# Kernel optimization log

Measured on AMD Instinct MI355X. Metric: run time of the kernel, lower is better.

## Reference

```python
import math
import jax, jax.numpy as jnp
import numpy as np

L, NH, DF = 4, 4, 32  # num_layers, num_heads, head_dim (H=128)
EPS = 1e-5


def ln(x, g, b):
    m = x.mean(-1, keepdims=True)
    v = ((x - m) ** 2).mean(-1, keepdims=True)
    return (x - m) * jax.lax.rsqrt(v + EPS) * g + b


def mha(x, w_in, b_in, w_out, b_out):
    # torch nn.MultiheadAttention self-attention, batch_first, no mask
    B, S, H = x.shape
    q, k, v = jnp.split(x @ w_in + b_in, 3, axis=-1)
    q = q.reshape(B, S, NH, DF)
    k = k.reshape(B, S, NH, DF)
    v = v.reshape(B, S, NH, DF)
    s = jnp.einsum('bqhd,bkhd->bhqk', q, k) / math.sqrt(DF)
    a = jax.nn.softmax(s, axis=-1)
    o = jnp.einsum('bhqk,bkhd->bqhd', a, v).reshape(B, S, H)
    return o @ w_out + b_out


def _forward(X_k, time_embed, step_embed, W_tr, b_tr, W_in, b_in, g_in, be_in,
             W_e, b_e, aw, ab, ow, ob, tng, tnb, f1w, f1b, f2w, f2b, fng, fnb,
             Wq, Wk, Wv, Wo, bo, Wem, bem, Wea, bea, e1w, e1b, e2w, e2b,
             gng, gnb, eng, enb, W_out, b_out, k_index, edge_index):
    B, N, T1, Cin = X_k.shape
    H = W_in.shape[1]
    # --- precompute_graph: self-loops + structural edge features ---
    loop = jnp.arange(N, dtype=edge_index.dtype)
    ei = jnp.concatenate([edge_index, jnp.stack([loop, loop])], axis=1)
    dst, src = ei[0], ei[1]
    E = ei.shape[1]
    deg = jnp.zeros((N,), jnp.float32).at[dst].add(1.0)
    deg_max = jnp.maximum(deg.max(), 1.0)
    edge_w = 1.0 / jnp.maximum(deg[dst], 1.0)
    feat = jnp.stack([edge_w, deg[src] / deg_max, deg[dst] / deg_max], axis=1)  # [E,3]
    # --- input embedding ---
    t_emb = time_embed  # [T1, te] (lookup of arange(T1) = whole table)
    X = jnp.concatenate(
        [X_k, jnp.broadcast_to(t_emb[None, None], (B, N, T1, t_emb.shape[-1]))], axis=-1)
    h = ln(X @ W_in + b_in, g_in, be_in)
    h = h + step_embed[k_index][:, None, None, :]
    e = feat @ W_e + b_e                       # [E, de]
    t_re = t_emb @ W_tr + b_tr                 # [T1, H]
    BT = B * T1
    for l in range(L):
        # temporal attention over T1
        h_flat = h.reshape(B * N, T1, H)
        attn_out = mha(h_flat, aw[l], ab[l], ow[l], ob[l])
        h = ln(h + attn_out.reshape(B, N, T1, H), tng[l], tnb[l])
        ffn = jax.nn.gelu(h @ f1w[l] + f1b[l], approximate=False) @ f2w[l] + f2b[l]
        h = ln(h + ffn, fng[l], fnb[l])
        h = h + t_re[None, None]
        # DiGress GT sparse graph block over N
        h_BT = h.transpose(0, 2, 1, 3).reshape(BT, N, H)
        Q = (h_BT @ Wq[l]).reshape(BT, N, NH, DF)
        K = (h_BT @ Wk[l]).reshape(BT, N, NH, DF)
        V = (h_BT @ Wv[l]).reshape(BT, N, NH, DF)
        scores = (Q[:, dst] * K[:, src]).sum(-1) / math.sqrt(DF)  # [BT,E,NH]
        scores = scores * (e @ Wem[l] + bem[l] + 1.0) + (e @ Wea[l] + bea[l])
        s_max = jax.lax.stop_gradient(scores.max(axis=1, keepdims=True))
        exp_s = jnp.exp(scores - s_max)
        denom = jnp.zeros((BT, N, NH), exp_s.dtype).at[:, dst, :].add(exp_s)
        attn = exp_s / (denom[:, dst, :] + 1e-9)
        agg = (attn[..., None] * V[:, src]).reshape(BT, E, H)
        out = jnp.zeros((BT, N, H), h.dtype).at[:, dst, :].add(agg)
        h_BT = h_BT + out @ Wo[l] + bo[l]
        h_mean = jax.lax.stop_gradient(h_BT).mean(0)               # [N,H]
        e_in = jnp.concatenate([h_mean[dst], h_mean[src], e], axis=-1)
        e_mlp = jax.nn.gelu(e_in @ e1w[l] + e1b[l], approximate=False) @ e2w[l] + e2b[l]
        e = ln(e + e_mlp, eng[l], enb[l])
        h = ln(h_BT.reshape(B, T1, N, H).transpose(0, 2, 1, 3), gng[l], gnb[l])
    return jax.nn.softmax(h @ W_out + b_out, axis=-1)


def setup_inputs() -> dict:
    key = jax.random.key(0)
    B, N, T1 = 2, 2000, 12
    sd, cc, te, H, de, nh = 4, 2, 16, 128, 16, 4
    Cin = (1 + cc) * sd  # 12
    E0, max_steps = 32000, 1024
    ks = iter(jax.random.split(key, 60))
    def rn(*shape, s=0.05):
        return jax.random.normal(next(ks), shape, jnp.float32) * s
    z = lambda *s: jnp.zeros(s, jnp.float32)
    o = lambda *s: jnp.ones(s, jnp.float32)
    return dict(
        X_k=jax.random.normal(next(ks), (B, N, T1, Cin), jnp.float32),
        time_embed=rn(T1, te), step_embed=rn(max_steps, H),
        W_tr=rn(te, H), b_tr=z(H),
        W_in=rn(Cin + te, H), b_in=z(H), g_in=o(H), be_in=z(H),
        W_e=rn(3, de), b_e=z(de),
        aw=rn(L, H, 3 * H), ab=z(L, 3 * H), ow=rn(L, H, H), ob=z(L, H),
        tng=o(L, H), tnb=z(L, H),
        f1w=rn(L, H, 2 * H), f1b=z(L, 2 * H), f2w=rn(L, 2 * H, H), f2b=z(L, H),
        fng=o(L, H), fnb=z(L, H),
        Wq=rn(L, H, H), Wk=rn(L, H, H), Wv=rn(L, H, H),
        Wo=rn(L, H, H), bo=z(L, H),
        Wem=rn(L, de, nh), bem=z(L, nh), Wea=rn(L, de, nh), bea=z(L, nh),
        e1w=rn(L, 2 * H + de, 4 * de), e1b=z(L, 4 * de),
        e2w=rn(L, 4 * de, de), e2b=z(L, de),
        gng=o(L, H), gnb=z(L, H), eng=o(L, de), enb=z(L, de),
        W_out=rn(H, sd), b_out=z(sd),
        k_index=jax.random.randint(next(ks), (B,), 0, max_steps),
        edge_index=jax.random.randint(next(ks), (2, E0), 0, N),
    )


def reference(X_k, time_embed, step_embed, W_tr, b_tr, W_in, b_in, g_in, be_in,
              W_e, b_e, aw, ab, ow, ob, tng, tnb, f1w, f1b, f2w, f2b, fng, fnb,
              Wq, Wk, Wv, Wo, bo, Wem, bem, Wea, bea, e1w, e1b, e2w, e2b,
              gng, gnb, eng, enb, W_out, b_out, k_index, edge_index):
    return _forward(X_k, time_embed, step_embed, W_tr, b_tr, W_in, b_in, g_in, be_in,
                    W_e, b_e, aw, ab, ow, ob, tng, tnb, f1w, f1b, f2w, f2b, fng, fnb,
                    Wq, Wk, Wv, Wo, bo, Wem, bem, Wea, bea, e1w, e1b, e2w, e2b,
                    gng, gnb, eng, enb, W_out, b_out, k_index, edge_index)
```

## Files before the change

kernel.cpp:

```cpp
#include <hip/hip_runtime.h>
#include <math.h>

#define NN 2000
#define T1C 12
#define BBC 2
#define HHC 128
#define NHD 4
#define DFD 32
#define LLC 4
#define DEC 16
#define TEC 16
#define CINC 12
#define E0C 32000
#define EEC 34000
#define BTC 24
#define MROWS 48000
#define EPSLN 1e-5f
#define SCALEQK 0.17677669529663687f

typedef __attribute__((ext_vector_type(8))) short short8;
typedef __attribute__((ext_vector_type(4))) float f32x4;


__device__ __forceinline__ unsigned short f2b(float f)
{
    unsigned u = __float_as_uint(f);
    return (unsigned short)((u + 0x7FFF + ((u >> 16) & 1)) >> 16);
}

__device__ __forceinline__ float b2f(unsigned short h)
{
    return __uint_as_float(((unsigned)h) << 16);
}


__global__ __launch_bounds__(256) void convwp_k(const float* __restrict__ W, unsigned short* __restrict__ Bp,
                                                int LN_, int K, int N, int noff, int Ntot)
{
    int idx = blockIdx.x * blockDim.x + threadIdx.x;
    int total = LN_ * K * N;
    if (idx >= total) return;
    int l = idx / (K * N);
    int r = idx - l * (K * N);
    int k = r / N;
    int n = r - k * N + noff;
    size_t off = (size_t)l * K * Ntot +
                 ((size_t)((n >> 4) * (K >> 5) + (k >> 5)) << 9) +
                 (((k >> 3) & 3) << 7) + ((n & 15) << 3) + (k & 7);
    Bp[off] = f2b(W[idx]);
}

__global__ __launch_bounds__(256) void convw12_k(const float* __restrict__ e1w, unsigned short* __restrict__ W12P)
{
    int idx = blockIdx.x * blockDim.x + threadIdx.x;
    if (idx >= LLC * 128 * 128) return;
    int l = idx >> 14;
    int r = idx & 16383;
    int c = r >> 7, k = r & 127;
    int sk = (c < 64) ? k : k + 128;
    int sc = c & 63;
    W12P[idx] = f2b(e1w[((size_t)l * 272 + sk) * 64 + sc]);
}

__global__ __launch_bounds__(256) void convwoT_k(const float* __restrict__ Wo, unsigned short* __restrict__ WoT)
{
    int idx = blockIdx.x * blockDim.x + threadIdx.x;
    if (idx >= LLC * 128 * 128) return;
    int l = idx >> 14;
    int r = idx & 16383;
    int c = r >> 7, k = r & 127;
    WoT[idx] = f2b(Wo[((size_t)l * 128 + k) * 128 + c]);
}


template<int K, int EPI, int OUTM>
__global__ __launch_bounds__(256) void gemm2_k(
    const unsigned short* __restrict__ A, const unsigned short* __restrict__ Bp,
    const float* __restrict__ bias, float* __restrict__ C, unsigned short* __restrict__ Cb,
    const float* __restrict__ res, const float* __restrict__ gam, const float* __restrict__ bet,
    const float* __restrict__ trep,
    int M, int Ntot)
{
    __shared__ unsigned short A_s[128 * 16 * 8];
    __shared__ float red2[2][128][2];

    int tid = threadIdx.x;
    int w = tid >> 6, lane = tid & 63;
    int wr = w & 1, wc = w >> 1;
    int quad = lane >> 4, lr = lane & 15;

    const unsigned short* abase = A + (size_t)blockIdx.x * 128 * K;
    int ntg0 = blockIdx.y * 8 + wc * 4;

    f32x4 acc[4][4];
#pragma unroll
    for (int mt = 0; mt < 4; mt++)
#pragma unroll
        for (int nt = 0; nt < 4; nt++) acc[mt][nt] = (f32x4){0.f, 0.f, 0.f, 0.f};

#pragma unroll
    for (int kb = 0; kb < K; kb += 128) {
        if (kb) __syncthreads();
#pragma unroll
        for (int j = 0; j < 8; j++) {
            int s = j * 256 + tid;
            int row = s >> 4, ks = s & 15;
            int ko = ks ^ (row & 15);
            uint4 d = *(const uint4*)(abase + (size_t)row * K + kb + ko * 8);
            *(uint4*)(A_s + s * 8) = d;
        }
        __syncthreads();
#pragma unroll
        for (int k0 = 0; k0 < 128; k0 += 32) {
            short8 af[4], bf[4];
#pragma unroll
            for (int mt = 0; mt < 4; mt++) {
                int row_l = wr * 64 + mt * 16 + lr;
                int koct = (k0 >> 3) + quad;
                int slot = row_l * 16 + (koct ^ lr);
                af[mt] = *(const short8*)(A_s + slot * 8);
            }
#pragma unroll
            for (int nt = 0; nt < 4; nt++) {
                size_t off = ((size_t)(ntg0 + nt) * (K >> 5) + ((kb + k0) >> 5)) * 512 + lane * 8;
                bf[nt] = *(const short8*)(Bp + off);
            }
#pragma unroll
            for (int mt = 0; mt < 4; mt++)
#pragma unroll
                for (int nt = 0; nt < 4; nt++)
                    acc[mt][nt] = __builtin_amdgcn_mfma_f32_16x16x32_bf16(af[mt], bf[nt], acc[mt][nt], 0, 0, 0);
        }
    }

    int rbase = blockIdx.x * 128 + wr * 64;
    int cbase = blockIdx.y * 128 + wc * 64;

    if constexpr (EPI != 3 && EPI != 4 && EPI != 5) {
#pragma unroll
        for (int mt = 0; mt < 4; mt++) {
#pragma unroll
            for (int nt = 0; nt < 4; nt++) {
                int colg = cbase + nt * 16 + lr;
                float bv = bias ? bias[colg] : 0.f;
#pragma unroll
                for (int i = 0; i < 4; i++) {
                    int row = rbase + mt * 16 + quad * 4 + i;
                    float x = acc[mt][nt][i] + bv;
                    if constexpr (EPI == 1) x = 0.5f * x * (1.f + erff(x * 0.70710678118654752f));
                    if constexpr (EPI == 2) x = res[(size_t)row * Ntot + colg] + x;
                    if constexpr (OUTM & 1) C[(size_t)row * Ntot + colg] = x;
                    if constexpr (OUTM & 4)
                        Cb[(size_t)blockIdx.y * M * 128 + (size_t)row * 128 + (wc * 64 + nt * 16 + lr)] = f2b(x);
                    else if constexpr (OUTM & 2)
                        Cb[(size_t)row * Ntot + colg] = f2b(x);
                }
            }
        }
    } else {
        float s[4][4], s2l[4][4];
#pragma unroll
        for (int mt = 0; mt < 4; mt++)
#pragma unroll
            for (int i = 0; i < 4; i++) { s[mt][i] = 0.f; s2l[mt][i] = 0.f; }
#pragma unroll
        for (int mt = 0; mt < 4; mt++) {
#pragma unroll
            for (int nt = 0; nt < 4; nt++) {
                int colg = cbase + nt * 16 + lr;
                float bv = bias[colg];
#pragma unroll
                for (int i = 0; i < 4; i++) {
                    int row = rbase + mt * 16 + quad * 4 + i;
                    float x = acc[mt][nt][i] + bv + res[(size_t)row * 128 + colg];
                    acc[mt][nt][i] = x;
                    s[mt][i] += x;
                    s2l[mt][i] += x * x;
                }
            }
        }
#pragma unroll
        for (int m = 1; m < 16; m <<= 1) {
#pragma unroll
            for (int mt = 0; mt < 4; mt++)
#pragma unroll
                for (int i = 0; i < 4; i++) {
                    s[mt][i]  += __shfl_xor(s[mt][i], m, 64);
                    s2l[mt][i] += __shfl_xor(s2l[mt][i], m, 64);
                }
        }
        if (lr == 0) {
#pragma unroll
            for (int mt = 0; mt < 4; mt++)
#pragma unroll
                for (int i = 0; i < 4; i++) {
                    int rl = wr * 64 + mt * 16 + quad * 4 + i;
                    red2[wc][rl][0] = s[mt][i];
                    red2[wc][rl][1] = s2l[mt][i];
                }
        }
        __syncthreads();
#pragma unroll
        for (int mt = 0; mt < 4; mt++) {
#pragma unroll
            for (int i = 0; i < 4; i++) {
                int rl = wr * 64 + mt * 16 + quad * 4 + i;
                float st  = red2[0][rl][0] + red2[1][rl][0];
                float s2t = red2[0][rl][1] + red2[1][rl][1];
                float mu = st * (1.f / 128.f);
                float rstd = rsqrtf(s2t * (1.f / 128.f) - mu * mu + EPSLN);
                int row = rbase + mt * 16 + quad * 4 + i;
                if constexpr (EPI == 4) {
                    int t = row % T1C;
                    int bn = row / T1C;
                    int b = bn / NN;
                    int n = bn - b * NN;
                    size_t rowp = (size_t)(b * T1C + t) * NN + n;
                    const float* trow = trep + t * HHC;
#pragma unroll
                    for (int nt = 0; nt < 4; nt++) {
                        int colg = cbase + nt * 16 + lr;
                        float y = (acc[mt][nt][i] - mu) * rstd * gam[colg] + bet[colg] + trow[colg];
                        C[rowp * 128 + colg] = y;
                        Cb[rowp * 128 + colg] = f2b(y);
                    }
                } else if constexpr (EPI == 5) {
                    int bt = row / NN, n = row - bt * NN;
                    int b = bt / T1C, t = bt - b * T1C;
                    size_t rowp = ((size_t)(b * NN + n)) * T1C + t;
#pragma unroll
                    for (int nt = 0; nt < 4; nt++) {
                        int colg = cbase + nt * 16 + lr;
                        float y = (acc[mt][nt][i] - mu) * rstd * gam[colg] + bet[colg];
                        C[rowp * 128 + colg] = y;
                        Cb[rowp * 128 + colg] = f2b(y);
                    }
                } else {
#pragma unroll
                    for (int nt = 0; nt < 4; nt++) {
                        int colg = cbase + nt * 16 + lr;
                        float y = (acc[mt][nt][i] - mu) * rstd * gam[colg] + bet[colg];
                        if constexpr (OUTM & 1) C[(size_t)row * 128 + colg] = y;
                        if constexpr (OUTM & 2) Cb[(size_t)row * 128 + colg] = f2b(y);
                    }
                }
            }
        }
    }
}

template<int K, int EPI, int OUTM>
static void run_gemm2(const unsigned short* A, const unsigned short* Bp, const float* bias,
                      float* C, unsigned short* Cb, const float* res, const float* g, const float* be,
                      const float* trep, int M, int Ntot, hipStream_t stream)
{
    dim3 grid(M / 128, Ntot / 128);
    gemm2_k<K, EPI, OUTM><<<grid, 256, 0, stream>>>(A, Bp, bias, C, Cb, res, g, be, trep, M, Ntot);
}


__global__ __launch_bounds__(256) void offn_k(
    const unsigned short* __restrict__ A,
    const unsigned short* __restrict__ Wp,
    const float* __restrict__ ob_l,
    const float* __restrict__ resh,
    const float* __restrict__ tng_l, const float* __restrict__ tnb_l,
    const unsigned short* __restrict__ F1p,
    const unsigned short* __restrict__ F2p,
    const float* __restrict__ f1b_l, const float* __restrict__ f2b_l,
    const float* __restrict__ fng_l, const float* __restrict__ fnb_l,
    const float* __restrict__ trep,
    float* __restrict__ C, unsigned short* __restrict__ Cb)
{
    __shared__ unsigned short A_s[32 * 16 * 8];
    __shared__ unsigned short M_s[32 * 16 * 8];
    __shared__ float red2[2][32][2];

    int tid = threadIdx.x;
    int w = tid >> 6, lane = tid & 63;
    int wr = w & 1, wc = w >> 1;
    int quad = lane >> 4, lr = lane & 15;

    const unsigned short* abase = A + (size_t)blockIdx.x * 32 * 128;

#pragma unroll
    for (int j = 0; j < 2; j++) {
        int s = j * 256 + tid;
        int row = s >> 4, ks = s & 15;
        int ko = ks ^ (row & 15);
        uint4 d = *(const uint4*)(abase + (size_t)row * 128 + ko * 8);
        *(uint4*)(A_s + s * 8) = d;
    }
    __syncthreads();

    f32x4 wacc[4];
#pragma unroll
    for (int nt = 0; nt < 4; nt++) wacc[nt] = (f32x4){0.f, 0.f, 0.f, 0.f};
#pragma unroll
    for (int k0 = 0; k0 < 128; k0 += 32) {
        int row_l = wr * 16 + lr;
        int koct = (k0 >> 3) + quad;
        int slot = row_l * 16 + (koct ^ lr);
        short8 af = *(const short8*)(A_s + slot * 8);
        short8 bf[4];
#pragma unroll
        for (int nt = 0; nt < 4; nt++) {
            size_t off = ((size_t)(wc * 4 + nt) * 4 + (k0 >> 5)) * 512 + lane * 8;
            bf[nt] = *(const short8*)(Wp + off);
        }
#pragma unroll
        for (int nt = 0; nt < 4; nt++)
            wacc[nt] = __builtin_amdgcn_mfma_f32_16x16x32_bf16(af, bf[nt], wacc[nt], 0, 0, 0);
    }

    int rbase = blockIdx.x * 32 + wr * 16;
    int cbase = wc * 64;

    float yv[4][4];
    {
        float s1[4], s2v[4];
#pragma unroll
        for (int i = 0; i < 4; i++) { s1[i] = 0.f; s2v[i] = 0.f; }
#pragma unroll
        for (int nt = 0; nt < 4; nt++) {
            int colg = cbase + nt * 16 + lr;
            float bv = ob_l[colg];
#pragma unroll
            for (int i = 0; i < 4; i++) {
                int row = rbase + quad * 4 + i;
                float x = wacc[nt][i] + bv + resh[(size_t)row * 128 + colg];
                yv[nt][i] = x;
                s1[i] += x;
                s2v[i] += x * x;
            }
        }
#pragma unroll
        for (int m = 1; m < 16; m <<= 1) {
#pragma unroll
            for (int i = 0; i < 4; i++) {
                s1[i]  += __shfl_xor(s1[i], m, 64);
                s2v[i] += __shfl_xor(s2v[i], m, 64);
            }
        }
        if (lr == 0) {
#pragma unroll
            for (int i = 0; i < 4; i++) {
                int rl = wr * 16 + quad * 4 + i;
                red2[wc][rl][0] = s1[i];
                red2[wc][rl][1] = s2v[i];
            }
        }
        __syncthreads();
#pragma unroll
        for (int i = 0; i < 4; i++) {
            int rl = wr * 16 + quad * 4 + i;
            float st  = red2[0][rl][0] + red2[1][rl][0];
            float s2t = red2[0][rl][1] + red2[1][rl][1];
            float mu = st * (1.f / 128.f);
            float rstd = rsqrtf(s2t * (1.f / 128.f) - mu * mu + EPSLN);
            int row = wr * 16 + quad * 4 + i;
#pragma unroll
            for (int nt = 0; nt < 4; nt++) {
                int col = cbase + nt * 16 + lr;
                float y = (yv[nt][i] - mu) * rstd * tng_l[col] + tnb_l[col];
                yv[nt][i] = y;
                int cchunk = col >> 3, celem = col & 7;
                int ks = cchunk ^ (row & 15);
                A_s[(row * 16 + ks) * 8 + celem] = f2b(y);
            }
        }
    }
    __syncthreads();

    f32x4 facc[4];
#pragma unroll
    for (int nt = 0; nt < 4; nt++) facc[nt] = (f32x4){0.f, 0.f, 0.f, 0.f};

#pragma unroll
    for (int half = 0; half < 2; half++) {
        f32x4 macc[4];
#pragma unroll
        for (int nt = 0; nt < 4; nt++) macc[nt] = (f32x4){0.f, 0.f, 0.f, 0.f};
#pragma unroll
        for (int k0 = 0; k0 < 128; k0 += 32) {
            int row_l = wr * 16 + lr;
            int koct = (k0 >> 3) + quad;
            int slot = row_l * 16 + (koct ^ lr);
            short8 af = *(const short8*)(A_s + slot * 8);
            short8 bf[4];
#pragma unroll
            for (int nt = 0; nt < 4; nt++) {
                size_t off = ((size_t)(half * 8 + wc * 4 + nt) * 4 + (k0 >> 5)) * 512 + lane * 8;
                bf[nt] = *(const short8*)(F1p + off);
            }
#pragma unroll
            for (int nt = 0; nt < 4; nt++)
                macc[nt] = __builtin_amdgcn_mfma_f32_16x16x32_bf16(af, bf[nt], macc[nt], 0, 0, 0);
        }
        if (half) __syncthreads();
#pragma unroll
        for (int nt = 0; nt < 4; nt++) {
            int col = wc * 64 + nt * 16 + lr;
            float bv = f1b_l[half * 128 + col];
            int cchunk = col >> 3, celem = col & 7;
#pragma unroll
            for (int i = 0; i < 4; i++) {
                int row = wr * 16 + quad * 4 + i;
                float x = macc[nt][i] + bv;
                x = 0.5f * x * (1.f + erff(x * 0.70710678118654752f));
                int ks = cchunk ^ (row & 15);
                M_s[(row * 16 + ks) * 8 + celem] = f2b(x);
            }
        }
        __syncthreads();
#pragma unroll
        for (int k0 = 0; k0 < 128; k0 += 32) {
            int row_l = wr * 16 + lr;
            int koct = (k0 >> 3) + quad;
            int slot = row_l * 16 + (koct ^ lr);
            short8 af = *(const short8*)(M_s + slot * 8);
            short8 bf[4];
#pragma unroll
            for (int nt = 0; nt < 4; nt++) {
                size_t off = ((size_t)(wc * 4 + nt) * 8 + ((half * 128 + k0) >> 5)) * 512 + lane * 8;
                bf[nt] = *(const short8*)(F2p + off);
            }
#pragma unroll
            for (int nt = 0; nt < 4; nt++)
                facc[nt] = __builtin_amdgcn_mfma_f32_16x16x32_bf16(af, bf[nt], facc[nt], 0, 0, 0);
        }
    }

    float s[4], s2l[4];
#pragma unroll
    for (int i = 0; i < 4; i++) { s[i] = 0.f; s2l[i] = 0.f; }
#pragma unroll
    for (int nt = 0; nt < 4; nt++) {
        int colg = cbase + nt * 16 + lr;
        float bv = f2b_l[colg];
#pragma unroll
        for (int i = 0; i < 4; i++) {
            float x = facc[nt][i] + bv + yv[nt][i];
            facc[nt][i] = x;
            s[i] += x;
            s2l[i] += x * x;
        }
    }
#pragma unroll
    for (int m = 1; m < 16; m <<= 1) {
#pragma unroll
        for (int i = 0; i < 4; i++) {
            s[i]  += __shfl_xor(s[i], m, 64);
            s2l[i] += __shfl_xor(s2l[i], m, 64);
        }
    }
    if (lr == 0) {
#pragma unroll
        for (int i = 0; i < 4; i++) {
            int rl = wr * 16 + quad * 4 + i;
            red2[wc][rl][0] = s[i];
            red2[wc][rl][1] = s2l[i];
        }
    }
    __syncthreads();
#pragma unroll
    for (int i = 0; i < 4; i++) {
        int rl = wr * 16 + quad * 4 + i;
        float st  = red2[0][rl][0] + red2[1][rl][0];
        float s2t = red2[0][rl][1] + red2[1][rl][1];
        float mu = st * (1.f / 128.f);
        float rstd = rsqrtf(s2t * (1.f / 128.f) - mu * mu + EPSLN);
        int row = rbase + quad * 4 + i;
        int t = row % T1C;
        int bn = row / T1C;
        int b = bn / NN;
        int n = bn - b * NN;
        size_t rowp = (size_t)(b * T1C + t) * NN + n;
        const float* trow = trep + t * HHC;
#pragma unroll
        for (int nt = 0; nt < 4; nt++) {
            int colg = cbase + nt * 16 + lr;
            float y = (facc[nt][i] - mu) * rstd * fng_l[colg] + fnb_l[colg] + trow[colg];
            C[rowp * 128 + colg] = y;
            Cb[rowp * 128 + colg] = f2b(y);
        }
    }
}


template<int NT>
__global__ __launch_bounds__(256) void gemm_mfma_k(
    const unsigned short* __restrict__ A, const unsigned short* __restrict__ WT,
    float* __restrict__ C, int M, int K)
{
    const int Nc = NT * 32;
    int tid = threadIdx.x;
    int w = tid >> 6, lane = tid & 63;
    int wr = w & 1, wc = w >> 1;
    int r0 = blockIdx.x * 32 + wr * 16;
    int c0 = wc * NT * 16;
    int lr = lane & 15;
    int kq = (lane >> 4) * 8;
    int arow = r0 + lr; if (arow >= M) arow = M - 1;
    const unsigned short* ap = A + (size_t)arow * K + kq;
    const unsigned short* wp = WT + (size_t)(c0 + lr) * K + kq;

    f32x4 acc[NT];
#pragma unroll
    for (int t = 0; t < NT; t++) acc[t] = (f32x4){0.f, 0.f, 0.f, 0.f};

    for (int k0 = 0; k0 < K; k0 += 32) {
        short8 a = *(const short8*)(ap + k0);
#pragma unroll
        for (int t = 0; t < NT; t++) {
            short8 b = *(const short8*)(wp + (size_t)t * 16 * K + k0);
            acc[t] = __builtin_amdgcn_mfma_f32_16x16x32_bf16(a, b, acc[t], 0, 0, 0);
        }
    }

    int orow0 = r0 + (lane >> 4) * 4;
#pragma unroll
    for (int t = 0; t < NT; t++) {
        int col = c0 + t * 16 + lr;
#pragma unroll
        for (int i = 0; i < 4; i++) {
            int row = orow0 + i;
            if (row < M) C[(size_t)row * Nc + col] = acc[t][i];
        }
    }
}

__global__ __launch_bounds__(256) void gemm_hm_k(
    const unsigned short* __restrict__ A, const unsigned short* __restrict__ WT,
    const float* __restrict__ mA, const float* __restrict__ bo,
    unsigned short* __restrict__ hmb, int M, int K)
{
    const int NT = 4;
    int tid = threadIdx.x;
    int w = tid >> 6, lane = tid & 63;
    int wr = w & 1, wc = w >> 1;
    int r0 = blockIdx.x * 32 + wr * 16;
    int c0 = wc * NT * 16;
    int lr = lane & 15;
    int kq = (lane >> 4) * 8;
    int arow = r0 + lr; if (arow >= M) arow = M - 1;
    const unsigned short* ap = A + (size_t)arow * K + kq;
    const unsigned short* wp = WT + (size_t)(c0 + lr) * K + kq;

    f32x4 acc[NT];
#pragma unroll
    for (int t = 0; t < NT; t++) acc[t] = (f32x4){0.f, 0.f, 0.f, 0.f};

    for (int k0 = 0; k0 < K; k0 += 32) {
        short8 a = *(const short8*)(ap + k0);
#pragma unroll
        for (int t = 0; t < NT; t++) {
            short8 b = *(const short8*)(wp + (size_t)t * 16 * K + k0);
            acc[t] = __builtin_amdgcn_mfma_f32_16x16x32_bf16(a, b, acc[t], 0, 0, 0);
        }
    }

    int orow0 = r0 + (lane >> 4) * 4;
#pragma unroll
    for (int t = 0; t < NT; t++) {
        int col = c0 + t * 16 + lr;
#pragma unroll
        for (int i = 0; i < 4; i++) {
            int row = orow0 + i;
            if (row < M) {
                float x = acc[t][i] + mA[(size_t)row * 128 + col] + bo[col];
                hmb[(size_t)row * 128 + col] = f2b(x);
            }
        }
    }
}


__global__ __launch_bounds__(256) void emlp_k(const float* __restrict__ P12,
                                              const int* __restrict__ dst, const int* __restrict__ src,
                                              const float* __restrict__ e1wE, const float* __restrict__ e1b_l,
                                              const float* __restrict__ e2w_l, const float* __restrict__ e2b_l,
                                              const float* __restrict__ g, const float* __restrict__ be,
                                              float* __restrict__ e)
{
    __shared__ float tl[4][64];
    int wv = threadIdx.x >> 6, l = threadIdx.x & 63;
    int r = blockIdx.x * 4 + wv;
    int d = dst[r], s = src[r];
    const float* ep = e + (size_t)r * DEC;
    float t = P12[(size_t)d * 128 + l] + P12[(size_t)s * 128 + 64 + l] + e1b_l[l];
#pragma unroll
    for (int k = 0; k < DEC; k++) t += ep[k] * e1wE[k * 64 + l];
    t = 0.5f * t * (1.f + erff(t * 0.70710678118654752f));
    tl[wv][l] = t;
    __syncthreads();
    int c = l & 15, kq = l >> 4;
    float p = 0.f;
#pragma unroll
    for (int j = 0; j < 16; j++) p += tl[wv][kq * 16 + j] * e2w_l[(kq * 16 + j) * 16 + c];
    p += __shfl_xor(p, 16, 64);
    p += __shfl_xor(p, 32, 64);
    float x = p + e2b_l[c] + ep[c];
    float s1 = x, s2 = x * x;
#pragma unroll
    for (int m = 1; m < 16; m <<= 1) {
        s1 += __shfl_xor(s1, m, 64);
        s2 += __shfl_xor(s2, m, 64);
    }
    float mu = s1 * (1.f / 16.f);
    float rstd = rsqrtf(s2 * (1.f / 16.f) - mu * mu + EPSLN);
    float y = (x - mu) * rstd * g[c] + be[c];
    if (l < 16) e[(size_t)r * DEC + c] = y;
}


__global__ __launch_bounds__(256) void zero_deg_k(int* __restrict__ degi)
{
    int i = blockIdx.x * blockDim.x + threadIdx.x;
    if (i < NN) degi[i] = 0;
}

__global__ __launch_bounds__(256) void build_edges_k(const int* __restrict__ eidx,
                                                     int* __restrict__ dst, int* __restrict__ src,
                                                     int* __restrict__ degi)
{
    int e = blockIdx.x * blockDim.x + threadIdx.x;
    if (e >= EEC) return;
    int d, s;
    if (e < E0C) { d = eidx[e]; s = eidx[E0C + e]; }
    else { d = e - E0C; s = e - E0C; }
    dst[e] = d;
    src[e] = s;
    atomicAdd(&degi[d], 1);
}

__global__ __launch_bounds__(256) void scan_k(const int* __restrict__ degi, int* __restrict__ rowptr,
                                              int* __restrict__ cursor, float* __restrict__ degmaxf)
{
    __shared__ int ssum[256];
    __shared__ int smx[256];
    int tid = threadIdx.x;
    int vals[8];
    int s = 0, mx = 0;
    int base = tid * 8;
#pragma unroll
    for (int j = 0; j < 8; j++) {
        int idx = base + j;
        int v = (idx < NN) ? degi[idx] : 0;
        vals[j] = v; s += v; mx = max(mx, v);
    }
    ssum[tid] = s; smx[tid] = mx;
    __syncthreads();
    for (int off = 1; off < 256; off <<= 1) {
        int t = (tid >= off) ? ssum[tid - off] : 0;
        __syncthreads();
        ssum[tid] += t;
        __syncthreads();
    }
    for (int off = 128; off > 0; off >>= 1) {
        if (tid < off) smx[tid] = max(smx[tid], smx[tid + off]);
        __syncthreads();
    }
    if (tid == 0) *degmaxf = fmaxf((float)smx[0], 1.f);
    int running = ssum[tid] - s;
#pragma unroll
    for (int j = 0; j < 8; j++) {
        int idx = base + j;
        if (idx < NN) { rowptr[idx] = running; cursor[idx] = running; running += vals[j]; }
    }
    if (tid == 255) rowptr[NN] = ssum[255];
}

__global__ __launch_bounds__(256) void feat_k(const int* __restrict__ dst, const int* __restrict__ src,
                                              const int* __restrict__ degi, const float* __restrict__ degmaxf,
                                              int* __restrict__ cursor, int* __restrict__ srcCSR,
                                              int* __restrict__ epos,
                                              const float* __restrict__ We, const float* __restrict__ bE,
                                              float* __restrict__ e)
{
    int ei = blockIdx.x * blockDim.x + threadIdx.x;
    if (ei >= EEC) return;
    int d = dst[ei], s = src[ei];
    int pos = atomicAdd(&cursor[d], 1);
    srcCSR[pos] = s;
    epos[ei] = pos;
    float dm = *degmaxf;
    float degd = (float)degi[d], degs = (float)degi[s];
    float f0 = 1.f / fmaxf(degd, 1.f);
    float f1 = degs / dm, f2 = degd / dm;
#pragma unroll
    for (int c = 0; c < DEC; c++)
        e[ei * DEC + c] = bE[c] + f0 * We[c] + f1 * We[DEC + c] + f2 * We[2 * DEC + c];
}


__global__ __launch_bounds__(256) void embed_k(const float* __restrict__ Xk, const float* __restrict__ temb,
                                               const float* __restrict__ Win, const float* __restrict__ bin,
                                               const float* __restrict__ g, const float* __restrict__ be,
                                               const float* __restrict__ stepemb, const int* __restrict__ kidx,
                                               float* __restrict__ h, unsigned short* __restrict__ hb)
{
    int row = blockIdx.x * 4 + (threadIdx.x >> 6);
    int l = threadIdx.x & 63;
    int t = row % T1C;
    int bn = row / T1C;
    int b = bn / NN;
    const float* xk = Xk + (size_t)row * CINC;
    const float* tp = temb + t * TEC;
    float acc0 = bin[l], acc1 = bin[l + 64];
#pragma unroll
    for (int k = 0; k < CINC; k++) {
        float xv = xk[k];
        acc0 += xv * Win[k * HHC + l];
        acc1 += xv * Win[k * HHC + l + 64];
    }
#pragma unroll
    for (int k = 0; k < TEC; k++) {
        float xv = tp[k];
        acc0 += xv * Win[(CINC + k) * HHC + l];
        acc1 += xv * Win[(CINC + k) * HHC + l + 64];
    }
    float s = acc0 + acc1, s2 = acc0 * acc0 + acc1 * acc1;
#pragma unroll
    for (int m = 32; m >= 1; m >>= 1) {
        s  += __shfl_xor(s, m, 64);
        s2 += __shfl_xor(s2, m, 64);
    }
    float mu = s * (1.f / 128.f);
    float rstd = rsqrtf(s2 * (1.f / 128.f) - mu * mu + EPSLN);
    const float* se = stepemb + (size_t)kidx[b] * HHC;
    float v0 = (acc0 - mu) * rstd * g[l] + be[l] + se[l];
    float v1 = (acc1 - mu) * rstd * g[l + 64] + be[l + 64] + se[l + 64];
    size_t ob = (size_t)row * HHC;
    h[ob + l] = v0;
    h[ob + l + 64] = v1;
    hb[ob + l] = f2b(v0);
    hb[ob + l + 64] = f2b(v1);
}

__global__ __launch_bounds__(128) void tre_k(const float* __restrict__ temb, const float* __restrict__ Wtr,
                                             const float* __restrict__ btr, float* __restrict__ tre)
{
    int t = blockIdx.x, c = threadIdx.x;
    float acc = btr[c];
#pragma unroll
    for (int k = 0; k < TEC; k++) acc += temb[t * TEC + k] * Wtr[k * HHC + c];
    tre[t * HHC + c] = acc;
}


__global__ __launch_bounds__(128) void temporal_attn_k(const unsigned short* __restrict__ qkvb,
                                                       unsigned short* __restrict__ outb)
{
    int bn = blockIdx.x;
    __shared__ unsigned short qkv_s[T1C][408];
    __shared__ float s[NHD][T1C][T1C];
    int tid = threadIdx.x;
    int hh = tid >> 5, lane = tid & 31;
    const unsigned short* base = qkvb + (size_t)bn * T1C * 384;
    for (int cIdx = tid; cIdx < 576; cIdx += 128) {
        uint4 d = *(const uint4*)(base + cIdx * 8);
        int t = cIdx / 48;
        int c0 = (cIdx - t * 48) * 8;
        *(uint4*)(&qkv_s[t][c0]) = d;
    }
    __syncthreads();
    for (int idx = lane; idx < T1C * T1C; idx += 32) {
        int tq = idx / T1C, tk = idx - tq * T1C;
        const unsigned* qp = (const unsigned*)&qkv_s[tq][hh * 32];
        const unsigned* kp = (const unsigned*)&qkv_s[tk][128 + hh * 32];
        float acc = 0.f;
#pragma unroll
        for (int d = 0; d < 16; d++) {
            unsigned a = qp[d], b = kp[d];
            acc += __uint_as_float(a << 16) * __uint_as_float(b << 16);
            acc += __uint_as_float(a & 0xFFFF0000u) * __uint_as_float(b & 0xFFFF0000u);
        }
        s[hh][tq][tk] = acc * SCALEQK;
    }
    __syncthreads();
    if (tid < NHD * T1C) {
        int h2 = tid / T1C, tq = tid - h2 * T1C;
        float mx = -1e30f;
#pragma unroll
        for (int j = 0; j < T1C; j++) mx = fmaxf(mx, s[h2][tq][j]);
        float sum = 0.f;
#pragma unroll
        for (int j = 0; j < T1C; j++) { float ex = __expf(s[h2][tq][j] - mx); s[h2][tq][j] = ex; sum += ex; }
        float inv = 1.f / sum;
#pragma unroll
        for (int j = 0; j < T1C; j++) s[h2][tq][j] *= inv;
    }
    __syncthreads();
    int oc = hh * 32 + lane;
#pragma unroll
    for (int t = 0; t < T1C; t++) {
        float acc = 0.f;
#pragma unroll
        for (int tk = 0; tk < T1C; tk++) acc += s[hh][t][tk] * b2f(qkv_s[tk][256 + oc]);
        outb[((size_t)bn * T1C + t) * HHC + oc] = f2b(acc);
    }
}


__global__ __launch_bounds__(256) void emea_k(const float* __restrict__ e, const int* __restrict__ epos,
                                              const float* __restrict__ Wem, const float* __restrict__ bem,
                                              const float* __restrict__ Wea, const float* __restrict__ bea,
                                              float* __restrict__ ec)
{
    int r = blockIdx.x * blockDim.x + threadIdx.x;
    if (r >= EEC) return;
    float ev[DEC];
#pragma unroll
    for (int k = 0; k < DEC; k++) ev[k] = e[r * DEC + k];
    int pos = epos[r];
#pragma unroll
    for (int hh = 0; hh < NHD; hh++) {
        float a = bem[hh], b2 = bea[hh];
#pragma unroll
        for (int k = 0; k < DEC; k++) { a += ev[k] * Wem[k * NHD + hh]; b2 += ev[k] * Wea[k * NHD + hh]; }
        ec[(size_t)pos * 8 + hh * 2]     = (a + 1.f) * SCALEQK;
        ec[(size_t)pos * 8 + hh * 2 + 1] = b2;
    }
}

__global__ __launch_bounds__(256) void sagg_k(const unsigned short* __restrict__ Q,
                                              const unsigned short* __restrict__ K,
                                              const unsigned short* __restrict__ V,
                                              const int* __restrict__ rowptr, const int* __restrict__ srcCSR,
                                              const float* __restrict__ ec, unsigned short* __restrict__ outb)
{
    int wv = threadIdx.x >> 6;
    int lane = threadIdx.x & 63;
    int blk = blockIdx.x;
    int bt = blk % BTC;
    int n  = (blk / BTC) * 4 + wv;
    int cg = lane & 15;
    int es = lane >> 4;
    int hh = cg >> 2;
    size_t base = (size_t)bt * NN;
    uint4 qd = *(const uint4*)(Q + (base + n) * HHC + cg * 8);
    unsigned qv[4] = {qd.x, qd.y, qd.z, qd.w};
    float q[8];
#pragma unroll
    for (int jj = 0; jj < 4; jj++) {
        q[2 * jj]     = __uint_as_float(qv[jj] << 16);
        q[2 * jj + 1] = __uint_as_float(qv[jj] & 0xFFFF0000u);
    }
    int s0 = rowptr[n], s1 = rowptr[n + 1];
    float acc[8];
#pragma unroll
    for (int j = 0; j < 8; j++) acc[j] = 0.f;
    float den = 0.f;
    for (int i = s0 + es; i < s1; i += 4) {
        int sn = srcCSR[i];
        uint4 kd = *(const uint4*)(K + (base + sn) * HHC + cg * 8);
        uint4 vd = *(const uint4*)(V + (base + sn) * HHC + cg * 8);
        float2 c2 = *(const float2*)(ec + (size_t)i * 8 + hh * 2);
        unsigned kv[4] = {kd.x, kd.y, kd.z, kd.w};
        float p = 0.f;
#pragma unroll
        for (int jj = 0; jj < 4; jj++) {
            p += q[2 * jj]     * __uint_as_float(kv[jj] << 16);
            p += q[2 * jj + 1] * __uint_as_float(kv[jj] & 0xFFFF0000u);
        }
        p += __shfl_xor(p, 1, 64);
        p += __shfl_xor(p, 2, 64);
        float w = __expf(p * c2.x + c2.y);
        unsigned vv[4] = {vd.x, vd.y, vd.z, vd.w};
#pragma unroll
        for (int jj = 0; jj < 4; jj++) {
            acc[2 * jj]     += w * __uint_as_float(vv[jj] << 16);
            acc[2 * jj + 1] += w * __uint_as_float(vv[jj] & 0xFFFF0000u);
        }
        den += w;
    }
#pragma unroll
    for (int j = 0; j < 8; j++) {
        acc[j] += __shfl_xor(acc[j], 16, 64);
        acc[j] += __shfl_xor(acc[j], 32, 64);
    }
    den += __shfl_xor(den, 16, 64);
    den += __shfl_xor(den, 32, 64);
    if (es == 0) {
        float inv = den + 1e-9f;
        unsigned short r[8];
#pragma unroll
        for (int j = 0; j < 8; j++) r[j] = f2b(acc[j] / inv);
        *(uint4*)(outb + (base + n) * HHC + cg * 8) = *(uint4*)r;
    }
}

__global__ __launch_bounds__(128) void hmean2_k(const float* __restrict__ hBT,
                                                const unsigned short* __restrict__ aggb,
                                                float* __restrict__ mA, unsigned short* __restrict__ mBb)
{
    int n = blockIdx.x, c = threadIdx.x;
    float sA = 0.f, sB = 0.f;
#pragma unroll
    for (int bt = 0; bt < BTC; bt++) {
        size_t off = ((size_t)bt * NN + n) * HHC + c;
        sA += hBT[off];
        sB += b2f(aggb[off]);
    }
    mA[n * HHC + c] = sA * (1.f / BTC);
    mBb[n * HHC + c] = f2b(sB * (1.f / BTC));
}


__global__ __launch_bounds__(256) void out_k(const float* __restrict__ h, const float* __restrict__ Wout,
                                             const float* __restrict__ bout, float* __restrict__ out)
{
    int row = blockIdx.x * 4 + (threadIdx.x >> 6);
    int lane = threadIdx.x & 63;
    const float* hp = h + (size_t)row * HHC;
    float x0 = hp[lane], x1 = hp[lane + 64];
    float w00 = Wout[lane * 4 + 0], w01 = Wout[lane * 4 + 1];
    float w02 = Wout[lane * 4 + 2], w03 = Wout[lane * 4 + 3];
    float w10 = Wout[(lane + 64) * 4 + 0], w11 = Wout[(lane + 64) * 4 + 1];
    float w12 = Wout[(lane + 64) * 4 + 2], w13 = Wout[(lane + 64) * 4 + 3];
    float p0 = x0 * w00 + x1 * w10;
    float p1 = x0 * w01 + x1 * w11;
    float p2 = x0 * w02 + x1 * w12;
    float p3 = x0 * w03 + x1 * w13;
#pragma unroll
    for (int m = 32; m >= 1; m >>= 1) {
        p0 += __shfl_xor(p0, m, 64);
        p1 += __shfl_xor(p1, m, 64);
        p2 += __shfl_xor(p2, m, 64);
        p3 += __shfl_xor(p3, m, 64);
    }
    if (lane == 0) {
        float l0 = p0 + bout[0], l1 = p1 + bout[1], l2 = p2 + bout[2], l3 = p3 + bout[3];
        float mx = fmaxf(fmaxf(l0, l1), fmaxf(l2, l3));
        float e0 = __expf(l0 - mx), e1 = __expf(l1 - mx), e2 = __expf(l2 - mx), e3 = __expf(l3 - mx);
        float inv = 1.f / (e0 + e1 + e2 + e3);
        float4 o = {e0 * inv, e1 * inv, e2 * inv, e3 * inv};
        *(float4*)(out + (size_t)row * 4) = o;
    }
}


extern "C" void kernel_launch(void* const* d_in, const int* in_sizes, int n_in,
                              void* d_out, int out_size, void* d_ws, size_t ws_size,
                              hipStream_t stream)
{
    const float* Xk      = (const float*)d_in[0];
    const float* temb    = (const float*)d_in[1];
    const float* stepemb = (const float*)d_in[2];
    const float* Wtr     = (const float*)d_in[3];
    const float* btr     = (const float*)d_in[4];
    const float* Win     = (const float*)d_in[5];
    const float* bin     = (const float*)d_in[6];
    const float* gin     = (const float*)d_in[7];
    const float* bein    = (const float*)d_in[8];
    const float* We      = (const float*)d_in[9];
    const float* bE      = (const float*)d_in[10];
    const float* aw      = (const float*)d_in[11];
    const float* ab      = (const float*)d_in[12];
    const float* ow      = (const float*)d_in[13];
    const float* ob      = (const float*)d_in[14];
    const float* tng     = (const float*)d_in[15];
    const float* tnb     = (const float*)d_in[16];
    const float* f1w     = (const float*)d_in[17];
    const float* f1b     = (const float*)d_in[18];
    const float* f2w     = (const float*)d_in[19];
    const float* f2b_    = (const float*)d_in[20];
    const float* fng     = (const float*)d_in[21];
    const float* fnb     = (const float*)d_in[22];
    const float* Wq      = (const float*)d_in[23];
    const float* Wk      = (const float*)d_in[24];
    const float* Wv      = (const float*)d_in[25];
    const float* Wo      = (const float*)d_in[26];
    const float* bo      = (const float*)d_in[27];
    const float* Wem     = (const float*)d_in[28];
    const float* bem     = (const float*)d_in[29];
    const float* Wea     = (const float*)d_in[30];
    const float* bea     = (const float*)d_in[31];
    const float* e1w     = (const float*)d_in[32];
    const float* e1b     = (const float*)d_in[33];
    const float* e2w     = (const float*)d_in[34];
    const float* e2b     = (const float*)d_in[35];
    const float* gng     = (const float*)d_in[36];
    const float* gnb     = (const float*)d_in[37];
    const float* eng     = (const float*)d_in[38];
    const float* enb     = (const float*)d_in[39];
    const float* Wout    = (const float*)d_in[40];
    const float* bout    = (const float*)d_in[41];
    const int*   kidx    = (const int*)d_in[42];
    const int*   eidx    = (const int*)d_in[43];
    float* outp = (float*)d_out;

    char* wsp = (char*)d_ws;
    auto alloc = [&](size_t nbytes) -> void* {
        void* p = (void*)wsp;
        wsp += (nbytes + 255) & ~(size_t)255;
        return p;
    };
    float* h     = (float*)alloc((size_t)MROWS * HHC * 4);
    unsigned short* hb = (unsigned short*)alloc((size_t)MROWS * HHC * 2);
    float* hBT   = (float*)alloc((size_t)MROWS * HHC * 4);
    unsigned short* hBTb = (unsigned short*)alloc((size_t)MROWS * HHC * 2);
    float* bufC  = (float*)alloc((size_t)MROWS * 384 * 4);
    unsigned short* bufDb = (unsigned short*)alloc((size_t)MROWS * HHC * 2);
    float* ebuf  = (float*)alloc((size_t)EEC * DEC * 4);
    float* ec    = (float*)alloc((size_t)EEC * NHD * 2 * 4);
    float* P12   = (float*)alloc((size_t)NN * HHC * 4);
    float* mA    = (float*)alloc((size_t)NN * HHC * 4);
    unsigned short* mBb = (unsigned short*)alloc((size_t)NN * HHC * 2);
    unsigned short* hmb = (unsigned short*)alloc((size_t)NN * HHC * 2);
    float* tre   = (float*)alloc((size_t)T1C * HHC * 4);
    float* degmaxf = (float*)alloc(4);
    int* degi   = (int*)alloc((size_t)NN * 4);
    int* dst    = (int*)alloc((size_t)EEC * 4);
    int* srcA   = (int*)alloc((size_t)EEC * 4);
    int* srcCSR = (int*)alloc((size_t)EEC * 4);
    int* epos   = (int*)alloc((size_t)EEC * 4);
    int* rowptr = (int*)alloc((size_t)(NN + 1) * 4);
    int* cursor = (int*)alloc((size_t)NN * 4);
    unsigned short* awP   = (unsigned short*)alloc((size_t)LLC * 384 * 128 * 2);
    unsigned short* owP   = (unsigned short*)alloc((size_t)LLC * 128 * 128 * 2);
    unsigned short* f1P   = (unsigned short*)alloc((size_t)LLC * 256 * 128 * 2);
    unsigned short* f2P   = (unsigned short*)alloc((size_t)LLC * 128 * 256 * 2);
    unsigned short* WqkvP = (unsigned short*)alloc((size_t)LLC * 384 * 128 * 2);
    unsigned short* WoP   = (unsigned short*)alloc((size_t)LLC * 128 * 128 * 2);
    unsigned short* WoT   = (unsigned short*)alloc((size_t)LLC * 128 * 128 * 2);
    unsigned short* W12P  = (unsigned short*)alloc((size_t)LLC * 128 * 128 * 2);

    unsigned short* bufCb = (unsigned short*)bufC;
    unsigned short* Qc    = (unsigned short*)bufC;
    unsigned short* Kc    = Qc + (size_t)MROWS * HHC;
    unsigned short* Vc    = Kc + (size_t)MROWS * HHC;

    {
        auto cwp = [&](const float* W, unsigned short* Bp, int K, int N, int noff, int Ntot) {
            int total = LLC * K * N;
            convwp_k<<<(total + 255) / 256, 256, 0, stream>>>(W, Bp, LLC, K, N, noff, Ntot);
        };
        cwp(aw,  awP, 128, 384, 0, 384);
        cwp(ow,  owP, 128, 128, 0, 128);
        cwp(f1w, f1P, 128, 256, 0, 256);
        cwp(f2w, f2P, 256, 128, 0, 128);
        cwp(Wq,  WqkvP, 128, 128, 0,   384);
        cwp(Wk,  WqkvP, 128, 128, 128, 384);
        cwp(Wv,  WqkvP, 128, 128, 256, 384);
        cwp(Wo,  WoP, 128, 128, 0, 128);
        convwoT_k<<<(LLC * 128 * 128 + 255) / 256, 256, 0, stream>>>(Wo, WoT);
        convw12_k<<<(LLC * 128 * 128 + 255) / 256, 256, 0, stream>>>(e1w, W12P);
    }

    zero_deg_k<<<(NN + 255) / 256, 256, 0, stream>>>(degi);
    build_edges_k<<<(EEC + 255) / 256, 256, 0, stream>>>(eidx, dst, srcA, degi);
    scan_k<<<1, 256, 0, stream>>>(degi, rowptr, cursor, degmaxf);
    feat_k<<<(EEC + 255) / 256, 256, 0, stream>>>(dst, srcA, degi, degmaxf, cursor, srcCSR, epos, We, bE, ebuf);

    embed_k<<<MROWS / 4, 256, 0, stream>>>(Xk, temb, Win, bin, gin, bein, stepemb, kidx, h, hb);
    tre_k<<<T1C, 128, 0, stream>>>(temb, Wtr, btr, tre);

    for (int l = 0; l < LLC; l++) {
        const unsigned short* awP_l   = awP   + (size_t)l * 384 * 128;
        const unsigned short* owP_l   = owP   + (size_t)l * 128 * 128;
        const unsigned short* f1P_l   = f1P   + (size_t)l * 256 * 128;
        const unsigned short* f2P_l   = f2P   + (size_t)l * 128 * 256;
        const unsigned short* WqkvP_l = WqkvP + (size_t)l * 384 * 128;
        const unsigned short* WoP_l   = WoP   + (size_t)l * 128 * 128;
        const unsigned short* WoT_l   = WoT   + (size_t)l * 128 * 128;
        const unsigned short* W12P_l  = W12P  + (size_t)l * 128 * 128;
        const float* ab_l  = ab  + (size_t)l * 3 * HHC;
        const float* ob_l  = ob  + (size_t)l * HHC;
        const float* tng_l = tng + (size_t)l * HHC;
        const float* tnb_l = tnb + (size_t)l * HHC;
        const float* f1b_l = f1b + (size_t)l * 256;
        const float* f2b_l = f2b_ + (size_t)l * HHC;
        const float* fng_l = fng + (size_t)l * HHC;
        const float* fnb_l = fnb + (size_t)l * HHC;
        const float* bo_l  = bo  + (size_t)l * HHC;
        const float* Wem_l = Wem + (size_t)l * DEC * NHD;
        const float* bem_l = bem + (size_t)l * NHD;
        const float* Wea_l = Wea + (size_t)l * DEC * NHD;
        const float* bea_l = bea + (size_t)l * NHD;
        const float* e1wE_l = e1w + ((size_t)l * 272 + 256) * 64;
        const float* e1b_l = e1b + (size_t)l * 64;
        const float* e2w_l = e2w + (size_t)l * 64 * DEC;
        const float* e2b_l = e2b + (size_t)l * DEC;
        const float* gng_l = gng + (size_t)l * HHC;
        const float* gnb_l = gnb + (size_t)l * HHC;
        const float* eng_l = eng + (size_t)l * DEC;
        const float* enb_l = enb + (size_t)l * DEC;

        run_gemm2<128, 0, 2>(hb, awP_l, ab_l, nullptr, bufCb, nullptr, nullptr, nullptr, nullptr, MROWS, 384, stream);
        temporal_attn_k<<<BBC * NN, 128, 0, stream>>>(bufCb, bufDb);
        offn_k<<<MROWS / 32, 256, 0, stream>>>(bufDb, owP_l, ob_l, h, tng_l, tnb_l,
                                               f1P_l, f2P_l, f1b_l, f2b_l, fng_l, fnb_l,
                                               tre, hBT, hBTb);
        run_gemm2<128, 0, 4>(hBTb, WqkvP_l, nullptr, nullptr, Qc, nullptr, nullptr, nullptr, nullptr, MROWS, 384, stream);
        emea_k<<<(EEC + 255) / 256, 256, 0, stream>>>(ebuf, epos, Wem_l, bem_l, Wea_l, bea_l, ec);
        sagg_k<<<BTC * (NN / 4), 256, 0, stream>>>(Qc, Kc, Vc, rowptr, srcCSR, ec, bufDb);
        hmean2_k<<<NN, 128, 0, stream>>>(hBT, bufDb, mA, mBb);
        run_gemm2<128, 5, 3>(bufDb, WoP_l, bo_l, h, hb, hBT, gng_l, gnb_l, nullptr, MROWS, 128, stream);
        gemm_hm_k<<<(NN + 31) / 32, 256, 0, stream>>>(mBb, WoT_l, mA, bo_l, hmb, NN, 128);
        gemm_mfma_k<4><<<(NN + 31) / 32, 256, 0, stream>>>(hmb, W12P_l, P12, NN, 128);
        emlp_k<<<EEC / 4, 256, 0, stream>>>(P12, dst, srcA, e1wE_l, e1b_l, e2w_l, e2b_l, eng_l, enb_l, ebuf);
    }

    out_k<<<MROWS / 4, 256, 0, stream>>>(h, Wout, bout, outp);
}
```

Baseline: 991.3 us.

## Fuse temporal QKV projection GEMM into temporal attention kernel

```diff
diff --git a/kernel.cpp b/kernel.cpp
--- a/kernel.cpp
+++ b/kernel.cpp
@@ -259,6 +259,98 @@
 }
 
 
+__global__ __launch_bounds__(128) void qkvattn_k(
+    const unsigned short* __restrict__ hb,
+    const unsigned short* __restrict__ Wp,
+    const float* __restrict__ ab_l,
+    unsigned short* __restrict__ outb)
+{
+    __shared__ unsigned short A_s[16 * 16 * 8];
+    __shared__ unsigned short qkv_s[T1C][408];
+    __shared__ float s[NHD][T1C][T1C];
+
+    int bn = blockIdx.x;
+    int tid = threadIdx.x;
+    int w = tid >> 6, lane = tid & 63;
+    int quad = lane >> 4, lr = lane & 15;
+
+    const unsigned short* abase = hb + (size_t)bn * T1C * 128;
+    for (int idx = tid; idx < 16 * 16; idx += 128) {
+        int row = idx >> 4, ks = idx & 15;
+        int ko = ks ^ (row & 15);
+        uint4 d;
+        if (row < T1C) d = *(const uint4*)(abase + (size_t)row * 128 + ko * 8);
+        else d = (uint4){0u, 0u, 0u, 0u};
+        *(uint4*)(A_s + idx * 8) = d;
+    }
+    __syncthreads();
+
+    f32x4 acc[12];
+#pragma unroll
+    for (int nt = 0; nt < 12; nt++) acc[nt] = (f32x4){0.f, 0.f, 0.f, 0.f};
+#pragma unroll
+    for (int k0 = 0; k0 < 128; k0 += 32) {
+        int koct = (k0 >> 3) + quad;
+        int slot = lr * 16 + (koct ^ lr);
+        short8 af = *(const short8*)(A_s + slot * 8);
+#pragma unroll
+        for (int nt = 0; nt < 12; nt++) {
+            size_t off = ((size_t)(w * 12 + nt) * 4 + (k0 >> 5)) * 512 + lane * 8;
+            short8 bf = *(const short8*)(Wp + off);
+            acc[nt] = __builtin_amdgcn_mfma_f32_16x16x32_bf16(af, bf, acc[nt], 0, 0, 0);
+        }
+    }
+#pragma unroll
+    for (int nt = 0; nt < 12; nt++) {
+        int col = w * 192 + nt * 16 + lr;
+        float bv = ab_l[col];
+#pragma unroll
+        for (int i = 0; i < 4; i++) {
+            int row = quad * 4 + i;
+            if (row < T1C) qkv_s[row][col] = f2b(acc[nt][i] + bv);
+        }
+    }
+    __syncthreads();
+
+    int hh = tid >> 5, lane32 = tid & 31;
+    for (int idx = lane32; idx < T1C * T1C; idx += 32) {
+        int tq = idx / T1C, tk = idx - tq * T1C;
+        const unsigned* qp = (const unsigned*)&qkv_s[tq][hh * 32];
+        const unsigned* kp = (const unsigned*)&qkv_s[tk][128 + hh * 32];
+        float a = 0.f;
+#pragma unroll
+        for (int d = 0; d < 16; d++) {
+            unsigned av = qp[d], bvv = kp[d];
+            a += __uint_as_float(av << 16) * __uint_as_float(bvv << 16);
+            a += __uint_as_float(av & 0xFFFF0000u) * __uint_as_float(bvv & 0xFFFF0000u);
+        }
+        s[hh][tq][tk] = a * SCALEQK;
+    }
+    __syncthreads();
+    if (tid < NHD * T1C) {
+        int h2 = tid / T1C, tq = tid - h2 * T1C;
+        float mx = -1e30f;
+#pragma unroll
+        for (int j = 0; j < T1C; j++) mx = fmaxf(mx, s[h2][tq][j]);
+        float sum = 0.f;
+#pragma unroll
+        for (int j = 0; j < T1C; j++) { float ex = __expf(s[h2][tq][j] - mx); s[h2][tq][j] = ex; sum += ex; }
+        float inv = 1.f / sum;
+#pragma unroll
+        for (int j = 0; j < T1C; j++) s[h2][tq][j] *= inv;
+    }
+    __syncthreads();
+    int oc = hh * 32 + lane32;
+#pragma unroll
+    for (int t = 0; t < T1C; t++) {
+        float a = 0.f;
+#pragma unroll
+        for (int tk = 0; tk < T1C; tk++) a += s[hh][t][tk] * b2f(qkv_s[tk][256 + oc]);
+        outb[((size_t)bn * T1C + t) * HHC + oc] = f2b(a);
+    }
+}
+
+
 __global__ __launch_bounds__(256) void offn_k(
     const unsigned short* __restrict__ A,
     const unsigned short* __restrict__ Wp,
@@ -746,60 +838,6 @@
 #pragma unroll
     for (int k = 0; k < TEC; k++) acc += temb[t * TEC + k] * Wtr[k * HHC + c];
     tre[t * HHC + c] = acc;
-}
-
-
-__global__ __launch_bounds__(128) void temporal_attn_k(const unsigned short* __restrict__ qkvb,
-                                                       unsigned short* __restrict__ outb)
-{
-    int bn = blockIdx.x;
-    __shared__ unsigned short qkv_s[T1C][408];
-    __shared__ float s[NHD][T1C][T1C];
-    int tid = threadIdx.x;
-    int hh = tid >> 5, lane = tid & 31;
-    const unsigned short* base = qkvb + (size_t)bn * T1C * 384;
-    for (int cIdx = tid; cIdx < 576; cIdx += 128) {
-        uint4 d = *(const uint4*)(base + cIdx * 8);
-        int t = cIdx / 48;
-        int c0 = (cIdx - t * 48) * 8;
-        *(uint4*)(&qkv_s[t][c0]) = d;
-    }
-    __syncthreads();
-    for (int idx = lane; idx < T1C * T1C; idx += 32) {
-        int tq = idx / T1C, tk = idx - tq * T1C;
-        const unsigned* qp = (const unsigned*)&qkv_s[tq][hh * 32];
-        const unsigned* kp = (const unsigned*)&qkv_s[tk][128 + hh * 32];
-        float acc = 0.f;
-#pragma unroll
-        for (int d = 0; d < 16; d++) {
-            unsigned a = qp[d], b = kp[d];
-            acc += __uint_as_float(a << 16) * __uint_as_float(b << 16);
-            acc += __uint_as_float(a & 0xFFFF0000u) * __uint_as_float(b & 0xFFFF0000u);
-        }
-        s[hh][tq][tk] = acc * SCALEQK;
-    }
-    __syncthreads();
-    if (tid < NHD * T1C) {
-        int h2 = tid / T1C, tq = tid - h2 * T1C;
-        float mx = -1e30f;
-#pragma unroll
-        for (int j = 0; j < T1C; j++) mx = fmaxf(mx, s[h2][tq][j]);
-        float sum = 0.f;
-#pragma unroll
-        for (int j = 0; j < T1C; j++) { float ex = __expf(s[h2][tq][j] - mx); s[h2][tq][j] = ex; sum += ex; }
-        float inv = 1.f / sum;
-#pragma unroll
-        for (int j = 0; j < T1C; j++) s[h2][tq][j] *= inv;
-    }
-    __syncthreads();
-    int oc = hh * 32 + lane;
-#pragma unroll
-    for (int t = 0; t < T1C; t++) {
-        float acc = 0.f;
-#pragma unroll
-        for (int tk = 0; tk < T1C; tk++) acc += s[hh][t][tk] * b2f(qkv_s[tk][256 + oc]);
-        outb[((size_t)bn * T1C + t) * HHC + oc] = f2b(acc);
-    }
 }
 
 
@@ -1027,7 +1065,6 @@
     unsigned short* WoT   = (unsigned short*)alloc((size_t)LLC * 128 * 128 * 2);
     unsigned short* W12P  = (unsigned short*)alloc((size_t)LLC * 128 * 128 * 2);
 
-    unsigned short* bufCb = (unsigned short*)bufC;
     unsigned short* Qc    = (unsigned short*)bufC;
     unsigned short* Kc    = Qc + (size_t)MROWS * HHC;
     unsigned short* Vc    = Kc + (size_t)MROWS * HHC;
@@ -1088,8 +1125,7 @@
         const float* eng_l = eng + (size_t)l * DEC;
         const float* enb_l = enb + (size_t)l * DEC;
 
-        run_gemm2<128, 0, 2>(hb, awP_l, ab_l, nullptr, bufCb, nullptr, nullptr, nullptr, nullptr, MROWS, 384, stream);
-        temporal_attn_k<<<BBC * NN, 128, 0, stream>>>(bufCb, bufDb);
+        qkvattn_k<<<BBC * NN, 128, 0, stream>>>(hb, awP_l, ab_l, bufDb);
         offn_k<<<MROWS / 32, 256, 0, stream>>>(bufDb, owP_l, ob_l, h, tng_l, tnb_l,
                                                f1P_l, f2P_l, f1b_l, f2b_l, fng_l, fnb_l,
                                                tre, hBT, hBTb);
```

Measured after the change: 1.004 ms. No clear change (+1.3%).

## Fuse QKV projection GEMM into output-projection/FFN kernel epilogue

Applied to the files above, without the earlier changes.

```diff
diff --git a/kernel.cpp b/kernel.cpp
--- a/kernel.cpp
+++ b/kernel.cpp
@@ -270,7 +270,9 @@
     const float* __restrict__ f1b_l, const float* __restrict__ f2b_l,
     const float* __restrict__ fng_l, const float* __restrict__ fnb_l,
     const float* __restrict__ trep,
-    float* __restrict__ C, unsigned short* __restrict__ Cb)
+    const unsigned short* __restrict__ Wqkv,
+    float* __restrict__ C,
+    unsigned short* __restrict__ Qc, unsigned short* __restrict__ Kc, unsigned short* __restrict__ Vc)
 {
     __shared__ unsigned short A_s[32 * 16 * 8];
     __shared__ unsigned short M_s[32 * 16 * 8];
@@ -463,6 +465,7 @@
         }
     }
     __syncthreads();
+    size_t rowp4[4];
 #pragma unroll
     for (int i = 0; i < 4; i++) {
         int rl = wr * 16 + quad * 4 + i;
@@ -476,13 +479,53 @@
         int b = bn / NN;
         int n = bn - b * NN;
         size_t rowp = (size_t)(b * T1C + t) * NN + n;
+        rowp4[i] = rowp;
         const float* trow = trep + t * HHC;
+        int rloc = wr * 16 + quad * 4 + i;
 #pragma unroll
         for (int nt = 0; nt < 4; nt++) {
             int colg = cbase + nt * 16 + lr;
             float y = (facc[nt][i] - mu) * rstd * fng_l[colg] + fnb_l[colg] + trow[colg];
             C[rowp * 128 + colg] = y;
-            Cb[rowp * 128 + colg] = f2b(y);
+            int cchunk = colg >> 3, celem = colg & 7;
+            int ks = cchunk ^ (rloc & 15);
+            A_s[(rloc * 16 + ks) * 8 + celem] = f2b(y);
+        }
+    }
+    __syncthreads();
+
+#pragma unroll
+    for (int g3 = 0; g3 < 3; g3++) {
+        f32x4 qacc[4];
+#pragma unroll
+        for (int nt = 0; nt < 4; nt++) qacc[nt] = (f32x4){0.f, 0.f, 0.f, 0.f};
+#pragma unroll
+        for (int k0 = 0; k0 < 128; k0 += 32) {
+            int row_l = wr * 16 + lr;
+            int koct = (k0 >> 3) + quad;
+            int slot = row_l * 16 + (koct ^ lr);
+            short8 af = *(const short8*)(A_s + slot * 8);
+            short8 bf[4];
+#pragma unroll
+            for (int nt = 0; nt < 4; nt++) {
+                size_t off = ((size_t)(wc * 12 + g3 * 4 + nt) * 4 + (k0 >> 5)) * 512 + lane * 8;
+                bf[nt] = *(const short8*)(Wqkv + off);
+            }
+#pragma unroll
+            for (int nt = 0; nt < 4; nt++)
+                qacc[nt] = __builtin_amdgcn_mfma_f32_16x16x32_bf16(af, bf[nt], qacc[nt], 0, 0, 0);
+        }
+#pragma unroll
+        for (int nt = 0; nt < 4; nt++) {
+            int colg = wc * 192 + (g3 * 4 + nt) * 16 + lr;
+            unsigned short* dstbuf;
+            int col;
+            if (colg < 128)      { dstbuf = Qc; col = colg; }
+            else if (colg < 256) { dstbuf = Kc; col = colg - 128; }
+            else                 { dstbuf = Vc; col = colg - 256; }
+#pragma unroll
+            for (int i = 0; i < 4; i++)
+                dstbuf[rowp4[i] * 128 + col] = f2b(qacc[nt][i]);
         }
     }
 }
@@ -1092,8 +1135,7 @@
         temporal_attn_k<<<BBC * NN, 128, 0, stream>>>(bufCb, bufDb);
         offn_k<<<MROWS / 32, 256, 0, stream>>>(bufDb, owP_l, ob_l, h, tng_l, tnb_l,
                                                f1P_l, f2P_l, f1b_l, f2b_l, fng_l, fnb_l,
-                                               tre, hBT, hBTb);
-        run_gemm2<128, 0, 4>(hBTb, WqkvP_l, nullptr, nullptr, Qc, nullptr, nullptr, nullptr, nullptr, MROWS, 384, stream);
+                                               tre, WqkvP_l, hBT, Qc, Kc, Vc);
         emea_k<<<(EEC + 255) / 256, 256, 0, stream>>>(ebuf, epos, Wem_l, bem_l, Wea_l, bea_l, ec);
         sagg_k<<<BTC * (NN / 4), 256, 0, stream>>>(Qc, Kc, Vc, rowptr, srcCSR, ec, bufDb);
         hmean2_k<<<NN, 128, 0, stream>>>(hBT, bufDb, mA, mBb);
```

Result: no change. 972.8 us (median of 2 runs) (-1.9%).
